# Performance work log

Hardware: AMD Instinct MI355X
Metric: run time of the kernel (lower is better)

The kernel has to match this reference:

```python
import jax, jax.numpy as jnp
import numpy as np

N_EMBD = 1024
HEAD_SIZE = 64
B, T = 8, 4096


def setup_inputs() -> dict:
    key = jax.random.key(0)
    kx, kk, kq, kv = jax.random.split(key, 4)
    scale = 1.0 / np.sqrt(N_EMBD)
    x = jax.random.normal(kx, (B, T, N_EMBD), dtype=jnp.float32)
    # nn.Linear(N_EMBD, head_size, bias=False) weights, stored as [in, out] for x @ W
    W_k = jax.random.uniform(kk, (N_EMBD, HEAD_SIZE), dtype=jnp.float32, minval=-scale, maxval=scale)
    W_q = jax.random.uniform(kq, (N_EMBD, HEAD_SIZE), dtype=jnp.float32, minval=-scale, maxval=scale)
    W_v = jax.random.uniform(kv, (N_EMBD, HEAD_SIZE), dtype=jnp.float32, minval=-scale, maxval=scale)
    return {"x": x, "W_k": W_k, "W_q": W_q, "W_v": W_v}


def reference(x, W_k, W_q, W_v) -> jnp.ndarray:
    # x: [B,T,E]; projections to [B,T,H]
    k = jnp.einsum("bte,eh->bth", x, W_k)
    q = jnp.einsum("bte,eh->bth", x, W_q)
    v = jnp.einsum("bte,eh->bth", x, W_v)
    H = W_k.shape[1]
    scores = jnp.einsum("bth,bsh->bts", q, k) * (H ** -0.5)  # [B,T,T]
    Tlen = x.shape[1]
    causal = jnp.tril(jnp.ones((Tlen, Tlen), dtype=bool))
    scores = jnp.where(causal, scores, -jnp.inf)
    attn = jax.nn.softmax(scores, axis=-1)
    # dropout is identity in eval mode (deterministic reference)
    return jnp.einsum("bts,bsh->bth", attn, v)
```

## Files before the change

### kernel.cpp

```cpp
#include <hip/hip_runtime.h>
#include <hip/hip_bf16.h>
#include <math.h>


#define BB 8
#define TT 4096
#define EE 1024
#define HH 64
#define NSLOT 160
#define SLOTF 4160

typedef __attribute__((ext_vector_type(8))) short short8;
typedef __attribute__((ext_vector_type(4))) float floatx4;
typedef short8 __attribute__((may_alias)) short8_a;
typedef uint2 __attribute__((may_alias)) uint2_a;
typedef uint4 __attribute__((may_alias)) uint4_a;
typedef float4 __attribute__((may_alias)) float4_a;

#define GLDS(gp, lp)                                                     \
  __builtin_amdgcn_global_load_lds(                                      \
      (const __attribute__((address_space(1))) unsigned int*)(gp),       \
      (__attribute__((address_space(3))) unsigned int*)(lp), 16, 0, 0)

__device__ __forceinline__ unsigned short f2bf(float f) {
  union { float f; unsigned int u; } v; v.f = f;
  unsigned int r = v.u + 0x7fffu + ((v.u >> 16) & 1u);
  return (unsigned short)(r >> 16);
}
__device__ __forceinline__ unsigned int pk2(float a, float b) {
  unsigned int r;
  asm("v_cvt_pk_bf16_f32 %0, %1, %2" : "=v"(r) : "v"(a), "v"(b));
  return r;
}
__device__ __forceinline__ floatx4 fzero() {
  floatx4 z = {0.f, 0.f, 0.f, 0.f};
  return z;
}
__device__ __forceinline__ floatx4 mfma_bf16(short8 a, short8 b, floatx4 c) {
  return __builtin_amdgcn_mfma_f32_16x16x32_bf16(a, b, c, 0, 0, 0);
}
__device__ __forceinline__ short8 pack8(float4 a, float4 b) {
  union { unsigned int u[4]; short8 s; } r;
  r.u[0] = pk2(a.x, a.y);
  r.u[1] = pk2(a.z, a.w);
  r.u[2] = pk2(b.x, b.y);
  r.u[3] = pk2(b.z, b.w);
  return r.s;
}

__global__ __launch_bounds__(256) void wt_kernel(
    const float* __restrict__ Wk, const float* __restrict__ Wq,
    const float* __restrict__ Wv, unsigned short* __restrict__ wt3) {
  __shared__ float tile[64][65];
  const int m = blockIdx.y;
  const int eb = blockIdx.x;
  const float* W = (m == 0) ? Wk : ((m == 1) ? Wq : Wv);
  const int t = threadIdx.x;
  {
    const int r = t >> 2;
    const int c0 = (t & 3) * 16;
    const float* src = W + (size_t)(eb * 64 + r) * 64 + c0;
#pragma unroll
    for (int i = 0; i < 16; ++i) tile[r][c0 + i] = src[i];
  }
  __syncthreads();
  {
    const int h = t >> 2;
    const int e0 = (t & 3) * 16;
    unsigned int w[8];
#pragma unroll
    for (int i = 0; i < 8; ++i)
      w[i] = pk2(tile[e0 + 2 * i][h], tile[e0 + 2 * i + 1][h]);
    unsigned short* dst = wt3 + (size_t)(m * 64 + h) * EE + eb * 64 + e0;
    ((uint4_a*)dst)[0] = make_uint4(w[0], w[1], w[2], w[3]);
    ((uint4_a*)(dst + 8))[0] = make_uint4(w[4], w[5], w[6], w[7]);
  }
}

__global__ __launch_bounds__(256) void proj_kernel(
    const float* __restrict__ x, const unsigned short* __restrict__ wt3,
    unsigned short* __restrict__ kws, unsigned short* __restrict__ qws,
    unsigned short* __restrict__ vtws) {
  __shared__ unsigned short Bl[2][24][512];
  const int t = threadIdx.x;
  const int wv = t >> 6, lane = t & 63;
  const int l16 = lane & 15, quad = lane >> 4;
  const int mshalf = wv & 1;
  const int jbase = (wv >> 1) * 6;
  const size_t row0 = (size_t)blockIdx.x * 64;

  floatx4 acc[6][2];
#pragma unroll
  for (int j = 0; j < 6; ++j)
#pragma unroll
    for (int m2 = 0; m2 < 2; ++m2) acc[j][m2] = fzero();

  const float* xbase = x + (row0 + mshalf * 32 + l16) * EE + quad * 8;

  float4 ra[2][2][2], rb[2][2][2];
#pragma unroll
  for (int m2 = 0; m2 < 2; ++m2)
#pragma unroll
    for (int f = 0; f < 2; ++f)
#pragma unroll
      for (int g = 0; g < 2; ++g)
        ra[m2][f][g] = *(const float4_a*)(xbase + (size_t)m2 * 16 * EE + f * 32 + g * 4);

#define STAGE_B(buf, kc)                                                       \
  {                                                                            \
    _Pragma("unroll") for (int i = 0; i < 6; ++i) {                            \
      const int idx = wv * 6 + i;                                              \
      const int j = idx >> 1, f = idx & 1;                                     \
      const unsigned short* gp =                                               \
          wt3 + (size_t)(j * 16 + l16) * EE + (kc) + f * 32 + quad * 8;        \
      GLDS(gp, &Bl[buf][idx][0]);                                              \
    }                                                                          \
  }

  STAGE_B(0, 0);
  __syncthreads();

  for (int c = 0; c < 16; ++c) {
    const int cur = c & 1;
    if (c < 15) {
      STAGE_B(cur ^ 1, (c + 1) * 64);
#pragma unroll
      for (int m2 = 0; m2 < 2; ++m2)
#pragma unroll
        for (int f = 0; f < 2; ++f)
#pragma unroll
          for (int g = 0; g < 2; ++g)
            rb[m2][f][g] = *(const float4_a*)(xbase + (size_t)m2 * 16 * EE +
                                              (c + 1) * 64 + f * 32 + g * 4);
    }
    short8 af[2][2];
#pragma unroll
    for (int m2 = 0; m2 < 2; ++m2)
#pragma unroll
      for (int f = 0; f < 2; ++f) af[m2][f] = pack8(ra[m2][f][0], ra[m2][f][1]);
#pragma unroll
    for (int j = 0; j < 6; ++j)
#pragma unroll
      for (int f = 0; f < 2; ++f) {
        short8 bf = *(const short8_a*)&Bl[cur][(jbase + j) * 2 + f][lane * 8];
#pragma unroll
        for (int m2 = 0; m2 < 2; ++m2)
          acc[j][m2] = mfma_bf16(af[m2][f], bf, acc[j][m2]);
      }
#pragma unroll
    for (int m2 = 0; m2 < 2; ++m2)
#pragma unroll
      for (int f = 0; f < 2; ++f)
#pragma unroll
        for (int g = 0; g < 2; ++g) ra[m2][f][g] = rb[m2][f][g];
    __syncthreads();
  }
#undef STAGE_B

  const int b = (int)(row0 >> 12);
  const int tt0 = (int)(row0 & (TT - 1));
#pragma unroll
  for (int j = 0; j < 6; ++j) {
    const int jg = jbase + j;
    const int m = jg >> 2;
    const int h0 = (jg & 3) * 16;
#pragma unroll
    for (int m2 = 0; m2 < 2; ++m2) {
      floatx4 a = acc[j][m2];
      const int rbase = mshalf * 32 + m2 * 16 + quad * 4;
      if (m == 0) {
#pragma unroll
        for (int r = 0; r < 4; ++r)
          kws[(row0 + rbase + r) * HH + h0 + l16] = f2bf(a[r]);
      } else if (m == 1) {
#pragma unroll
        for (int r = 0; r < 4; ++r)
          qws[(row0 + rbase + r) * HH + h0 + l16] = f2bf(a[r] * 0.18033688011112042f);
      } else {
        uint2 p;
        p.x = pk2(a[0], a[1]);
        p.y = pk2(a[2], a[3]);
        ((uint2_a*)&vtws[(size_t)(b * 64 + h0 + l16) * TT + tt0 + rbase])[0] = p;
      }
    }
  }
}

template <bool SPLIT>
__global__ __launch_bounds__(256) void attn_kernel(
    const unsigned short* __restrict__ kws, const unsigned short* __restrict__ qws,
    const unsigned short* __restrict__ vtws, float* __restrict__ dst) {
  __shared__ unsigned short KV[2][16][512];
  __shared__ unsigned short pb[4][16][72];
  const int t = threadIdx.x;
  const int wv = t >> 6, lane = t & 63;
  const int l16 = lane & 15, quad = lane >> 4;
  const int id = (int)blockIdx.x;
  int b, jq, kt0, kt1;
  if (SPLIT) {
    b = id & 7;
    const int cid = id >> 3;
    int s, S;
    if (cid < 16) {
      jq = cid; s = 0; S = 1;
    } else if (cid < 48) {
      const int u = cid - 16; jq = 16 + (u >> 1); s = u & 1; S = 2;
    } else if (cid < 96) {
      const int u = cid - 48; const int d = u / 3; jq = 32 + d; s = u - 3 * d; S = 3;
    } else {
      const int u = cid - 96; jq = 48 + (u >> 2); s = u & 3; S = 4;
    }
    const int n = jq + 1;
    kt0 = (s * n) / S;
    kt1 = ((s + 1) * n) / S;
  } else {
    const int r255 = id & 255;
    b = r255 & 7;
    const int m = r255 >> 3;
    jq = (id < 256) ? m : 63 - m;
    kt0 = 0;
    kt1 = jq + 1;
  }
  const int q0 = jq * 64;
  const int qrow = q0 + wv * 16 + l16;

  const unsigned short* qp = qws + ((size_t)b * TT + qrow) * HH + quad * 8;
  short8 qa0 = *(const short8_a*)(qp);
  short8 qa1 = *(const short8_a*)(qp + 32);

  floatx4 o[4];
#pragma unroll
  for (int nt = 0; nt < 4; ++nt) o[nt] = fzero();
  float lsum = 0.f;

#define STAGE_KV(buf, ks)                                                      \
  {                                                                            \
    _Pragma("unroll") for (int i = 0; i < 4; ++i) {                            \
      const int idx = wv * 4 + i;                                              \
      const unsigned short* gp;                                                \
      if (idx < 8) {                                                           \
        const int nt = idx >> 1, f = idx & 1;                                  \
        gp = kws + ((size_t)b * TT + (ks) + nt * 16 + l16) * HH + f * 32 +     \
             quad * 8;                                                         \
      } else {                                                                 \
        const int nt = (idx - 8) >> 1, f = idx & 1;                            \
        gp = vtws + ((size_t)(b * 64 + nt * 16 + l16)) * TT + (ks) + f * 32 +  \
             quad * 8;                                                         \
      }                                                                        \
      GLDS(gp, &KV[buf][idx][0]);                                              \
    }                                                                          \
  }

  STAGE_KV(0, kt0 * 64);
  __syncthreads();

  for (int kt = kt0; kt < kt1; ++kt) {
    const int cur = (kt - kt0) & 1;
    const int ks = kt * 64;
    if (kt + 1 < kt1) STAGE_KV(cur ^ 1, ks + 64);

    floatx4 sc[4];
#pragma unroll
    for (int nt = 0; nt < 4; ++nt) {
      short8 kf0 = *(const short8_a*)&KV[cur][nt * 2][lane * 8];
      short8 kf1 = *(const short8_a*)&KV[cur][nt * 2 + 1][lane * 8];
      floatx4 z = fzero();
      z = mfma_bf16(kf0, qa0, z);
      z = mfma_bf16(kf1, qa1, z);
      sc[nt] = z;
    }
    if (kt == jq) {
#pragma unroll
      for (int nt = 0; nt < 4; ++nt)
#pragma unroll
        for (int r = 0; r < 4; ++r) {
          const int key = ks + nt * 16 + quad * 4 + r;
          if (key > qrow) sc[nt][r] = -1e30f;
        }
    }
#pragma unroll
    for (int nt = 0; nt < 4; ++nt) {
      const float p0 = exp2f(sc[nt][0]);
      const float p1 = exp2f(sc[nt][1]);
      const float p2 = exp2f(sc[nt][2]);
      const float p3 = exp2f(sc[nt][3]);
      lsum += (p0 + p1) + (p2 + p3);
      uint2 pw;
      pw.x = pk2(p0, p1);
      pw.y = pk2(p2, p3);
      ((uint2_a*)&pb[wv][l16][nt * 16 + quad * 4])[0] = pw;
    }
    short8 pf0 = *(const short8_a*)&pb[wv][l16][quad * 8];
    short8 pf1 = *(const short8_a*)&pb[wv][l16][quad * 8 + 32];
#pragma unroll
    for (int nt = 0; nt < 4; ++nt) {
      short8 vf0 = *(const short8_a*)&KV[cur][8 + nt * 2][lane * 8];
      short8 vf1 = *(const short8_a*)&KV[cur][8 + nt * 2 + 1][lane * 8];
      o[nt] = mfma_bf16(vf0, pf0, o[nt]);
      o[nt] = mfma_bf16(vf1, pf1, o[nt]);
    }
    __syncthreads();
  }
#undef STAGE_KV

  float lr = lsum;
  lr += __shfl_xor(lr, 16);
  lr += __shfl_xor(lr, 32);

  if (SPLIT) {
    float* op = dst + (size_t)id * SLOTF;
    const int ql = wv * 16 + l16;
#pragma unroll
    for (int nt = 0; nt < 4; ++nt) {
      float4 st;
      st.x = o[nt][0];
      st.y = o[nt][1];
      st.z = o[nt][2];
      st.w = o[nt][3];
      *(float4_a*)&op[(size_t)ql * 64 + nt * 16 + quad * 4] = st;
    }
    if (lane < 16) op[4096 + wv * 16 + lane] = lr;
  } else {
    const float inv = 1.0f / lr;
#pragma unroll
    for (int nt = 0; nt < 4; ++nt) {
      float4 st;
      st.x = o[nt][0] * inv;
      st.y = o[nt][1] * inv;
      st.z = o[nt][2] * inv;
      st.w = o[nt][3] * inv;
      *(float4_a*)&dst[((size_t)b * TT + qrow) * HH + nt * 16 + quad * 4] = st;
    }
  }
}

__global__ __launch_bounds__(256) void comb_kernel(
    const float* __restrict__ part, float* __restrict__ out) {
  const int id = (int)blockIdx.x;
  const int b = id & 7;
  const int jq = id >> 3;
  const int tq = jq >> 4;
  const int S = tq + 1;
  const int P = 8 * tq * (tq + 1) + (jq & 15) * S;
  const int t = threadIdx.x;
  const int r0 = t >> 6;
  const int h = t & 63;
  const float* s0 = part + (size_t)(b + 8 * P) * SLOTF;
  const size_t sstr = (size_t)8 * SLOTF;

#pragma unroll 4
  for (int i = 0; i < 16; ++i) {
    const int r = i * 4 + r0;
    float acc = 0.f, l = 0.f;
    for (int s2 = 0; s2 < S; ++s2) {
      acc += s0[(size_t)s2 * sstr + (size_t)r * 64 + h];
      l += s0[(size_t)s2 * sstr + 4096 + r];
    }
    out[((size_t)b * TT + jq * 64 + r) * HH + h] = acc / l;
  }
}

extern "C" void kernel_launch(void* const* d_in, const int* in_sizes, int n_in,
                              void* d_out, int out_size, void* d_ws, size_t ws_size,
                              hipStream_t stream) {
  const float* x = (const float*)d_in[0];
  const float* Wk = (const float*)d_in[1];
  const float* Wq = (const float*)d_in[2];
  const float* Wv = (const float*)d_in[3];
  float* out = (float*)d_out;

  unsigned short* kws = (unsigned short*)d_ws;
  unsigned short* qws = kws + (size_t)BB * TT * HH;
  unsigned short* vtws = qws + (size_t)BB * TT * HH;
  unsigned short* wt3 = vtws + (size_t)BB * TT * HH;
  float* part = (float*)(wt3 + (size_t)3 * HH * EE);

  const size_t base_bytes = (size_t)3 * BB * TT * HH * 2 + (size_t)3 * HH * EE * 2;
  const size_t need = base_bytes + (size_t)BB * NSLOT * SLOTF * 4;
  const bool use_split = (ws_size >= need);

  hipLaunchKernelGGL(wt_kernel, dim3(16, 3), dim3(256), 0, stream, Wk, Wq, Wv, wt3);
  hipLaunchKernelGGL(proj_kernel, dim3(512), dim3(256), 0, stream, x, wt3, kws, qws,
                     vtws);
  if (use_split) {
    hipLaunchKernelGGL((attn_kernel<true>), dim3(BB * NSLOT), dim3(256), 0, stream,
                       kws, qws, vtws, part);
    hipLaunchKernelGGL(comb_kernel, dim3(512), dim3(256), 0, stream, part, out);
  } else {
    hipLaunchKernelGGL((attn_kernel<false>), dim3(512), dim3(256), 0, stream,
                       kws, qws, vtws, out);
  }
}
```

Measured before the change: 289.8 us.

## Stage x tiles through LDS with triple-buffered async loads in projection kernel

The projection kernel now loads the fp32 x activations through global_load_lds into an XOR-swizzled LDS buffer together with the bf16 weight tiles, using a 3-deep ring of 32-wide K chunks. Previously x was prefetched into registers one chunk ahead. Explicit vmcnt waits and raw barriers keep two stages in flight to hide memory latency and reduce register pressure. The trade-off is more LDS use per block, a smaller K chunk per iteration with twice as many barriers, and hand-tuned waitcnt values that must exactly match the number of outstanding loads.

```diff
diff --git a/kernel.cpp b/kernel.cpp
--- a/kernel.cpp
+++ b/kernel.cpp
@@ -81,7 +81,7 @@
     const float* __restrict__ x, const unsigned short* __restrict__ wt3,
     unsigned short* __restrict__ kws, unsigned short* __restrict__ qws,
     unsigned short* __restrict__ vtws) {
-  __shared__ unsigned short Bl[2][24][512];
+  __shared__ __align__(16) unsigned char LB[3][20480];
   const int t = threadIdx.x;
   const int wv = t >> 6, lane = t & 63;
   const int l16 = lane & 15, quad = lane >> 4;
@@ -95,67 +95,73 @@
 #pragma unroll
     for (int m2 = 0; m2 < 2; ++m2) acc[j][m2] = fzero();
 
-  const float* xbase = x + (row0 + mshalf * 32 + l16) * EE + quad * 8;
-
-  float4 ra[2][2][2], rb[2][2][2];
-#pragma unroll
-  for (int m2 = 0; m2 < 2; ++m2)
-#pragma unroll
-    for (int f = 0; f < 2; ++f)
-#pragma unroll
-      for (int g = 0; g < 2; ++g)
-        ra[m2][f][g] = *(const float4_a*)(xbase + (size_t)m2 * 16 * EE + f * 32 + g * 4);
-
-#define STAGE_B(buf, kc)                                                       \
+  const int sg = (lane & 7) ^ ((lane >> 3) & 7);
+  const int arow = lane >> 3;
+
+#define STAGE(bufp, cc)                                                        \
   {                                                                            \
-    _Pragma("unroll") for (int i = 0; i < 6; ++i) {                            \
-      const int idx = wv * 6 + i;                                              \
-      const int j = idx >> 1, f = idx & 1;                                     \
-      const unsigned short* gp =                                               \
-          wt3 + (size_t)(j * 16 + l16) * EE + (kc) + f * 32 + quad * 8;        \
-      GLDS(gp, &Bl[buf][idx][0]);                                              \
+    _Pragma("unroll") for (int i = 0; i < 5; ++i) {                            \
+      const int q = wv * 5 + i;                                                \
+      if (q < 8) {                                                             \
+        const float* gp =                                                      \
+            x + (row0 + 8 * q + arow) * EE + (cc) * 32 + sg * 4;               \
+        GLDS(gp, (bufp) + q * 1024);                                           \
+      } else {                                                                 \
+        const int j = q - 8;                                                   \
+        const unsigned short* gp =                                             \
+            wt3 + (size_t)(j * 16 + l16) * EE + (cc) * 32 + quad * 8;          \
+        GLDS(gp, (bufp) + 8192 + j * 1024);                                    \
+      }                                                                        \
     }                                                                          \
   }
 
-  STAGE_B(0, 0);
-  __syncthreads();
-
-  for (int c = 0; c < 16; ++c) {
-    const int cur = c & 1;
-    if (c < 15) {
-      STAGE_B(cur ^ 1, (c + 1) * 64);
+  STAGE(&LB[0][0], 0);
+  STAGE(&LB[1][0], 1);
+  asm volatile("s_waitcnt vmcnt(5)" ::: "memory");
+  __builtin_amdgcn_s_barrier();
+  __builtin_amdgcn_sched_barrier(0);
+
+  int cur = 0;
+  for (int c = 0; c < 32; ++c) {
+    const unsigned char* Ab = &LB[cur][0];
+    float4 a4[2][2];
+#pragma unroll
+    for (int m2 = 0; m2 < 2; ++m2) {
+      const int row = mshalf * 32 + m2 * 16 + l16;
+#pragma unroll
+      for (int h = 0; h < 2; ++h) {
+        const int gsw = (quad * 2 + h) ^ (row & 7);
+        a4[m2][h] = *(const float4_a*)(Ab + row * 128 + gsw * 16);
+      }
+    }
+    if (c + 2 < 32) {
+      int sb = cur + 2;
+      if (sb >= 3) sb -= 3;
+      STAGE(&LB[sb][0], c + 2);
+    }
+    short8 af[2];
+#pragma unroll
+    for (int m2 = 0; m2 < 2; ++m2) af[m2] = pack8(a4[m2][0], a4[m2][1]);
+#pragma unroll
+    for (int jj = 0; jj < 6; ++jj) {
+      short8 bfv = *(const short8_a*)(Ab + 8192 + (size_t)(jbase + jj) * 1024 +
+                                      lane * 16);
 #pragma unroll
       for (int m2 = 0; m2 < 2; ++m2)
-#pragma unroll
-        for (int f = 0; f < 2; ++f)
-#pragma unroll
-          for (int g = 0; g < 2; ++g)
-            rb[m2][f][g] = *(const float4_a*)(xbase + (size_t)m2 * 16 * EE +
-                                              (c + 1) * 64 + f * 32 + g * 4);
-    }
-    short8 af[2][2];
-#pragma unroll
-    for (int m2 = 0; m2 < 2; ++m2)
-#pragma unroll
-      for (int f = 0; f < 2; ++f) af[m2][f] = pack8(ra[m2][f][0], ra[m2][f][1]);
-#pragma unroll
-    for (int j = 0; j < 6; ++j)
-#pragma unroll
-      for (int f = 0; f < 2; ++f) {
-        short8 bf = *(const short8_a*)&Bl[cur][(jbase + j) * 2 + f][lane * 8];
-#pragma unroll
-        for (int m2 = 0; m2 < 2; ++m2)
-          acc[j][m2] = mfma_bf16(af[m2][f], bf, acc[j][m2]);
+        acc[jj][m2] = mfma_bf16(af[m2], bfv, acc[jj][m2]);
+    }
+    if (c < 31) {
+      if (c <= 29) {
+        asm volatile("s_waitcnt vmcnt(5)" ::: "memory");
+      } else {
+        asm volatile("s_waitcnt vmcnt(0)" ::: "memory");
       }
-#pragma unroll
-    for (int m2 = 0; m2 < 2; ++m2)
-#pragma unroll
-      for (int f = 0; f < 2; ++f)
-#pragma unroll
-        for (int g = 0; g < 2; ++g) ra[m2][f][g] = rb[m2][f][g];
-    __syncthreads();
-  }
-#undef STAGE_B
+      __builtin_amdgcn_s_barrier();
+      __builtin_amdgcn_sched_barrier(0);
+    }
+    cur = (cur == 2) ? 0 : cur + 1;
+  }
+#undef STAGE
 
   const int b = (int)(row0 >> 12);
   const int tt0 = (int)(row0 & (TT - 1));
```

Measured after the change: 283.3 us. 1.02x faster.

## Load projection weights directly into registers instead of staging through LDS

Applied to the files above, without the earlier changes.

The projection kernel no longer stages weight tiles into shared memory with global_load_lds and barriers. Each wave now loads its own B fragments straight from global memory into registers, double-buffered with ping-pong register sets over 32-wide k chunks in a fully unrolled loop. This removes the LDS traffic and the per-iteration __syncthreads. In exchange, weight reads are redundant across waves (the two waves sharing a jbase read the same rows), and register pressure rises from the unrolled double buffers.

```diff
diff --git a/kernel.cpp b/kernel.cpp
--- a/kernel.cpp
+++ b/kernel.cpp
@@ -81,7 +81,6 @@
     const float* __restrict__ x, const unsigned short* __restrict__ wt3,
     unsigned short* __restrict__ kws, unsigned short* __restrict__ qws,
     unsigned short* __restrict__ vtws) {
-  __shared__ unsigned short Bl[2][24][512];
   const int t = threadIdx.x;
   const int wv = t >> 6, lane = t & 63;
   const int l16 = lane & 15, quad = lane >> 4;
@@ -96,66 +95,47 @@
     for (int m2 = 0; m2 < 2; ++m2) acc[j][m2] = fzero();
 
   const float* xbase = x + (row0 + mshalf * 32 + l16) * EE + quad * 8;
-
-  float4 ra[2][2][2], rb[2][2][2];
-#pragma unroll
-  for (int m2 = 0; m2 < 2; ++m2)
-#pragma unroll
-    for (int f = 0; f < 2; ++f)
-#pragma unroll
-      for (int g = 0; g < 2; ++g)
-        ra[m2][f][g] = *(const float4_a*)(xbase + (size_t)m2 * 16 * EE + f * 32 + g * 4);
-
-#define STAGE_B(buf, kc)                                                       \
+  const unsigned short* wbase = wt3 + ((size_t)jbase * 16 + l16) * EE + quad * 8;
+
+  float4 PA[2][2], QA[2][2];
+  short8 PB[6], QB[6];
+
+#define LOAD_A(DST, c)                                                         \
   {                                                                            \
-    _Pragma("unroll") for (int i = 0; i < 6; ++i) {                            \
-      const int idx = wv * 6 + i;                                              \
-      const int j = idx >> 1, f = idx & 1;                                     \
-      const unsigned short* gp =                                               \
-          wt3 + (size_t)(j * 16 + l16) * EE + (kc) + f * 32 + quad * 8;        \
-      GLDS(gp, &Bl[buf][idx][0]);                                              \
+    _Pragma("unroll") for (int m2 = 0; m2 < 2; ++m2)                           \
+    _Pragma("unroll") for (int h = 0; h < 2; ++h)                              \
+      DST[m2][h] = *(const float4_a*)(xbase + (size_t)m2 * 16 * EE +           \
+                                      (c) * 32 + h * 4);                       \
+  }
+#define LOAD_B(DST, c)                                                         \
+  {                                                                            \
+    _Pragma("unroll") for (int jj = 0; jj < 6; ++jj)                           \
+      DST[jj] = *(const short8_a*)(wbase + (size_t)jj * 16 * EE + (c) * 32);   \
+  }
+#define BODY(CA, CB, NA, NB, c)                                                \
+  {                                                                            \
+    if ((c) + 1 < 32) {                                                        \
+      LOAD_A(NA, (c) + 1);                                                     \
+      LOAD_B(NB, (c) + 1);                                                     \
     }                                                                          \
-  }
-
-  STAGE_B(0, 0);
-  __syncthreads();
-
-  for (int c = 0; c < 16; ++c) {
-    const int cur = c & 1;
-    if (c < 15) {
-      STAGE_B(cur ^ 1, (c + 1) * 64);
-#pragma unroll
-      for (int m2 = 0; m2 < 2; ++m2)
-#pragma unroll
-        for (int f = 0; f < 2; ++f)
-#pragma unroll
-          for (int g = 0; g < 2; ++g)
-            rb[m2][f][g] = *(const float4_a*)(xbase + (size_t)m2 * 16 * EE +
-                                              (c + 1) * 64 + f * 32 + g * 4);
-    }
-    short8 af[2][2];
-#pragma unroll
-    for (int m2 = 0; m2 < 2; ++m2)
-#pragma unroll
-      for (int f = 0; f < 2; ++f) af[m2][f] = pack8(ra[m2][f][0], ra[m2][f][1]);
-#pragma unroll
-    for (int j = 0; j < 6; ++j)
-#pragma unroll
-      for (int f = 0; f < 2; ++f) {
-        short8 bf = *(const short8_a*)&Bl[cur][(jbase + j) * 2 + f][lane * 8];
-#pragma unroll
-        for (int m2 = 0; m2 < 2; ++m2)
-          acc[j][m2] = mfma_bf16(af[m2][f], bf, acc[j][m2]);
-      }
-#pragma unroll
-    for (int m2 = 0; m2 < 2; ++m2)
-#pragma unroll
-      for (int f = 0; f < 2; ++f)
-#pragma unroll
-        for (int g = 0; g < 2; ++g) ra[m2][f][g] = rb[m2][f][g];
-    __syncthreads();
-  }
-#undef STAGE_B
+    short8 af[2];                                                              \
+    _Pragma("unroll") for (int m2 = 0; m2 < 2; ++m2)                           \
+      af[m2] = pack8(CA[m2][0], CA[m2][1]);                                    \
+    _Pragma("unroll") for (int jj = 0; jj < 6; ++jj)                           \
+    _Pragma("unroll") for (int m2 = 0; m2 < 2; ++m2)                           \
+      acc[jj][m2] = mfma_bf16(af[m2], CB[jj], acc[jj][m2]);                    \
+  }
+
+  LOAD_A(PA, 0);
+  LOAD_B(PB, 0);
+#pragma unroll
+  for (int cp = 0; cp < 16; ++cp) {
+    BODY(PA, PB, QA, QB, 2 * cp);
+    BODY(QA, QB, PA, PB, 2 * cp + 1);
+  }
+#undef BODY
+#undef LOAD_B
+#undef LOAD_A
 
   const int b = (int)(row0 >> 12);
   const int tt0 = (int)(row0 & (TT - 1));
```

Result: slower. 305.7 us (+5.5%).
